# Kernel tuning notes

Hardware: AMD Instinct MI355X
Metric: run time of the kernel (lower is better)

The kernel has to match this reference:

```python
import jax, jax.numpy as jnp
import numpy as np

B, E = 256, 512
C, K = 8192, 10          # n_class, n_center
LMD = 10.0
INV_GAMMA = 10.0         # 1 / gamma, gamma = 0.1
TAU = 0.2
MARGIN = 0.01


def setup_inputs() -> dict:
    key = jax.random.key(0)
    k1, k2, k3 = jax.random.split(key, 3)
    embeddings = jax.random.normal(k1, (B, E), dtype=jnp.float32)
    labels = jax.random.randint(k2, (B,), 0, C, dtype=jnp.int64)
    fc = jax.random.normal(k3, (C * K, E), dtype=jnp.float32)
    return {"embeddings": embeddings, "labels": labels, "fc": fc}


def reference(embeddings, labels, fc):
    # L2-normalize centers (rows of fc), like F.normalize(fc, p=2, dim=1)
    norm = jnp.sqrt(jnp.sum(fc * fc, axis=1, keepdims=True))
    w = fc / jnp.maximum(norm, 1e-12)

    # similarity to every center: [B, C, K]
    x = (embeddings @ w.T).reshape(B, C, K)
    prob = jax.nn.softmax(INV_GAMMA * x, axis=2)
    h = jnp.sum(prob * x, axis=2)  # [B, C] soft-pooled class similarity

    # subtract margin on ground-truth class, then cross-entropy
    rows = jnp.arange(B)
    margin_m = jnp.zeros_like(h).at[rows, labels].set(MARGIN)
    logits = LMD * (h - margin_m)
    logp = jax.nn.log_softmax(logits, axis=1)
    loss_cls = -jnp.mean(logp[rows, labels])

    # regularizer: batched per-class center gram, replaces python loop over C
    wc = w.reshape(C, K, E)
    sub = 1.0 - jnp.einsum('cke,cje->ckj', wc, wc)   # [C, K, K]
    sub = jnp.where(sub <= 0.0, 1e-10, sub)
    mask = jnp.triu(jnp.ones((K, K), dtype=bool), k=1)  # strict upper triangle
    safe = jnp.where(mask, 2.0 * sub, 1.0)
    reg = jnp.sum(jnp.where(mask, jnp.sqrt(safe), 0.0))
    reg = reg / (C * K * (K - 1.0))
    return loss_cls + TAU * reg
```

## Files before the change

kernel.cpp:

```cpp
#include <hip/hip_runtime.h>


typedef __bf16 bf16;
typedef bf16 bf16x8 __attribute__((ext_vector_type(8)));
typedef float f32x4 __attribute__((ext_vector_type(4)));

#define NCLASS 8192
#define KC 10
#define EDIM 512
#define BATCH 256
#define BK 64

__device__ inline void load_lds16(const void* g, void* l) {
    __builtin_amdgcn_global_load_lds(
        (const __attribute__((address_space(1))) void*)g,
        (__attribute__((address_space(3))) void*)l, 16, 0, 0);
}

__global__ __launch_bounds__(256) void prep_kernel(
    const float* __restrict__ fc, bf16* __restrict__ w,
    float* __restrict__ gram_part,
    const float* __restrict__ e, bf16* __restrict__ At,
    float* __restrict__ sumexp)
{
    __shared__ float rows[KC * EDIM];
    __shared__ float s_invn[KC];
    __shared__ float s_wsum[4];
    const int t = threadIdx.x;

    if (blockIdx.x >= NCLASS) {
        if (blockIdx.x == NCLASS + 64) {
            sumexp[t] = 0.0f;
            return;
        }
        int i = (blockIdx.x - NCLASS) * 256 + t;
        int row = i >> 6, chunk = i & 63;
        int k = chunk * 8;
        float4 a = ((const float4*)e)[i * 2];
        float4 b = ((const float4*)e)[i * 2 + 1];
        bf16x8 v;
        v[0] = (bf16)a.x; v[1] = (bf16)a.y; v[2] = (bf16)a.z; v[3] = (bf16)a.w;
        v[4] = (bf16)b.x; v[5] = (bf16)b.y; v[6] = (bf16)b.z; v[7] = (bf16)b.w;
        *(bf16x8*)&At[((k >> 5) << 13) + (row << 5) + (k & 31)] = v;
        return;
    }

    const int c = blockIdx.x;
    const int wave = t >> 6, lane = t & 63;

    const float4* src = (const float4*)(fc + (size_t)c * (KC * EDIM));
    float4* rows4 = (float4*)rows;
    #pragma unroll
    for (int i = 0; i < 5; ++i) rows4[t + i * 256] = src[t + i * 256];
    __syncthreads();

    for (int r = wave; r < KC; r += 4) {
        float s = 0.f;
        #pragma unroll
        for (int j = 0; j < 8; ++j) {
            float v = rows[r * EDIM + lane + j * 64];
            s += v * v;
        }
        #pragma unroll
        for (int off = 32; off; off >>= 1) s += __shfl_xor(s, off);
        if (lane == 0) s_invn[r] = 1.0f / fmaxf(sqrtf(s), 1e-12f);
    }
    __syncthreads();

    bf16x8* dst = (bf16x8*)(w + (size_t)c * (KC * EDIM));
    #pragma unroll
    for (int p = 0; p < 3; ++p) {
        int j = t + p * 256;
        if (j < 640) {
            int r = j >> 6;
            float inv = s_invn[r];
            float4 a = *(const float4*)(rows + j * 8);
            float4 b = *(const float4*)(rows + j * 8 + 4);
            bf16x8 v;
            v[0] = (bf16)(a.x * inv); v[1] = (bf16)(a.y * inv);
            v[2] = (bf16)(a.z * inv); v[3] = (bf16)(a.w * inv);
            v[4] = (bf16)(b.x * inv); v[5] = (bf16)(b.y * inv);
            v[6] = (bf16)(b.z * inv); v[7] = (bf16)(b.w * inv);
            dst[j] = v;
        }
    }

    float part = 0.f;
    for (int p = wave; p < 45; p += 4) {
        int i = 0, pp = p;
        while (pp >= 9 - i) { pp -= 9 - i; ++i; }
        int j = i + 1 + pp;
        float s = 0.f;
        #pragma unroll
        for (int u = 0; u < 8; ++u)
            s += rows[i * EDIM + lane + u * 64] * rows[j * EDIM + lane + u * 64];
        #pragma unroll
        for (int off = 32; off; off >>= 1) s += __shfl_xor(s, off);
        if (lane == 0) {
            float sub = 1.0f - s * s_invn[i] * s_invn[j];
            if (sub <= 0.0f) sub = 1e-10f;
            part += sqrtf(2.0f * sub);
        }
    }
    if (lane == 0) s_wsum[wave] = part;
    __syncthreads();
    if (t == 0) gram_part[c] = s_wsum[0] + s_wsum[1] + s_wsum[2] + s_wsum[3];
}

__global__ __launch_bounds__(512, 2) void gemm_h_kernel(
    const bf16* __restrict__ W,
    const bf16* __restrict__ At,
    const int* __restrict__ labels,
    float* __restrict__ sumexp,
    float* __restrict__ lab_logit)
{
    __shared__ bf16 Ws[2][80 * BK];
    const int tid = threadIdx.x;
    const int wave = tid >> 6, lane = tid & 63;

    f32x4 acc[5][2];
    #pragma unroll
    for (int mt = 0; mt < 5; ++mt)
        #pragma unroll
        for (int nt = 0; nt < 2; ++nt)
            acc[mt][nt] = (f32x4){0.f, 0.f, 0.f, 0.f};

    const size_t g0 = (size_t)blockIdx.x * 80;

    const int rA = tid >> 3, sA = tid & 7;
    const bf16* srcA = W + (g0 + rA) * EDIM + ((sA ^ (rA & 7)) << 3);
    const int rB = (512 + tid) >> 3, sB = tid & 7;
    const bf16* srcB = W + (g0 + rB) * EDIM + ((sB ^ (rB & 7)) << 3);

    const int q = lane >> 4;
    const int q8 = q * 8;
    const int fr = lane & 15;

    load_lds16(srcA, &Ws[0][wave * 512]);
    if (tid < 128) load_lds16(srcB, &Ws[0][4096 + wave * 512]);
    __syncthreads();

    for (int t = 0; t < 8; ++t) {
        const int cur = t & 1;
        if (t < 7) {
            const int kb = (t + 1) * BK;
            load_lds16(srcA + kb, &Ws[cur ^ 1][wave * 512]);
            if (tid < 128) load_lds16(srcB + kb, &Ws[cur ^ 1][4096 + wave * 512]);
        }
        #pragma unroll
        for (int kk = 0; kk < BK; kk += 32) {
            const int ccb = kk >> 3;
            bf16x8 wf[5], ef[2];
            #pragma unroll
            for (int nt = 0; nt < 2; ++nt) {
                int row = wave * 32 + nt * 16 + fr;
                ef[nt] = *(const bf16x8*)
                    &At[((t * 2 + (kk >> 5)) << 13) + (row << 5) + q8];
            }
            #pragma unroll
            for (int mt = 0; mt < 5; ++mt) {
                int row = mt * 16 + fr;
                int s = (ccb + q) ^ (row & 7);
                wf[mt] = *(const bf16x8*)&Ws[cur][row * BK + (s << 3)];
            }
            #pragma unroll
            for (int mt = 0; mt < 5; ++mt)
                #pragma unroll
                for (int nt = 0; nt < 2; ++nt)
                    acc[mt][nt] = __builtin_amdgcn_mfma_f32_16x16x32_bf16(
                        wf[mt], ef[nt], acc[mt][nt], 0, 0, 0);
        }
        __syncthreads();
    }

    const int col = lane & 15;
    const int quad = lane >> 4;
    const int cb = blockIdx.x * 8;
    #pragma unroll
    for (int nt = 0; nt < 2; ++nt) {
        int b = wave * 32 + nt * 16 + col;
        float hval[8];
        #pragma unroll
        for (int cc = 0; cc < 8; ++cc) {
            float xm = -1e30f;
            #pragma unroll
            for (int mt = 0; mt < 5; ++mt) {
                if (10 * cc + 10 > 16 * mt && 10 * cc < 16 * mt + 16) {
                    #pragma unroll
                    for (int rg = 0; rg < 4; ++rg) {
                        int r = 16 * mt + 4 * quad + rg;
                        if (r >= 10 * cc && r < 10 * cc + 10)
                            xm = fmaxf(xm, acc[mt][nt][rg]);
                    }
                }
            }
            xm = fmaxf(xm, __shfl_xor(xm, 16));
            xm = fmaxf(xm, __shfl_xor(xm, 32));
            float s1 = 0.f, s2 = 0.f;
            #pragma unroll
            for (int mt = 0; mt < 5; ++mt) {
                if (10 * cc + 10 > 16 * mt && 10 * cc < 16 * mt + 16) {
                    #pragma unroll
                    for (int rg = 0; rg < 4; ++rg) {
                        int r = 16 * mt + 4 * quad + rg;
                        if (r >= 10 * cc && r < 10 * cc + 10) {
                            float x = acc[mt][nt][rg];
                            float e = __expf(10.0f * (x - xm));
                            s1 += e; s2 += e * x;
                        }
                    }
                }
            }
            s1 += __shfl_xor(s1, 16); s1 += __shfl_xor(s1, 32);
            s2 += __shfl_xor(s2, 16); s2 += __shfl_xor(s2, 32);
            hval[cc] = s2 / s1;
        }
        if (quad == 0) {
            const int lbl = labels[b];
            float ps = 0.f;
            #pragma unroll
            for (int cc = 0; cc < 8; ++cc) {
                float lg = 10.0f * hval[cc];
                if (lbl == cb + cc) {
                    lg -= 0.1f;
                    lab_logit[b] = lg;
                }
                ps += __expf(lg);
            }
            atomicAdd(&sumexp[b], ps);
        }
    }
}

__global__ __launch_bounds__(256) void final_kernel(
    const float* __restrict__ gram_part, const float* __restrict__ sumexp,
    const float* __restrict__ lab_logit, float* __restrict__ out)
{
    __shared__ float red[4];
    const int t = threadIdx.x, wave = t >> 6, lane = t & 63;
    const float4* gp4 = (const float4*)gram_part;
    float g = 0.f;
    #pragma unroll
    for (int i = 0; i < 8; ++i) {
        float4 x = gp4[t + i * 256];
        g += x.x + x.y + x.z + x.w;
    }
    float ce = logf(sumexp[t]) - lab_logit[t];
    float val = ce * (1.0f / 256.0f)
              + g * (0.2f / 737280.0f);
    #pragma unroll
    for (int off = 32; off; off >>= 1) val += __shfl_xor(val, off);
    if (lane == 0) red[wave] = val;
    __syncthreads();
    if (t == 0) out[0] = red[0] + red[1] + red[2] + red[3];
}

extern "C" void kernel_launch(void* const* d_in, const int* in_sizes, int n_in,
                              void* d_out, int out_size, void* d_ws, size_t ws_size,
                              hipStream_t stream) {
    const float* emb    = (const float*)d_in[0];
    const int*   labels = (const int*)d_in[1];
    const float* fc     = (const float*)d_in[2];
    float* out = (float*)d_out;

    char* ws = (char*)d_ws;
    bf16*  w         = (bf16*)ws;
    bf16*  At        = (bf16*)(ws + 83886080);
    float* gram_part = (float*)(ws + 84148224);
    float* sumexp    = (float*)(ws + 84181248);
    float* lab_logit = (float*)(ws + 84182272);

    prep_kernel<<<NCLASS + 65, 256, 0, stream>>>(fc, w, gram_part, emb, At,
                                                 sumexp);
    gemm_h_kernel<<<81920 / 80, 512, 0, stream>>>(w, At, labels,
                                                  sumexp, lab_logit);
    final_kernel<<<1, 256, 0, stream>>>(gram_part, sumexp, lab_logit, out);
}
```

Baseline: 304.6 us.

## Assign one class per wave in prep kernel, keep center rows in registers

The prep kernel now gives each wave its own class instead of one class per 256-thread block. Each lane holds 8 floats of all 10 rows in registers and computes the norms and all 45 Gram dot products with wave shuffles, with no shared memory or block barriers. This removes LDS staging and __syncthreads overhead and shrinks the grid by four. The cost is higher register pressure (80 floats of row data per lane) and 45 serialized shuffle reductions per wave.

```diff
diff --git a/kernel.cpp b/kernel.cpp
--- a/kernel.cpp
+++ b/kernel.cpp
@@ -23,17 +23,14 @@
     const float* __restrict__ e, bf16* __restrict__ At,
     float* __restrict__ sumexp)
 {
-    __shared__ float rows[KC * EDIM];
-    __shared__ float s_invn[KC];
-    __shared__ float s_wsum[4];
     const int t = threadIdx.x;
 
-    if (blockIdx.x >= NCLASS) {
-        if (blockIdx.x == NCLASS + 64) {
+    if (blockIdx.x >= 2048) {
+        if (blockIdx.x == 2048 + 64) {
             sumexp[t] = 0.0f;
             return;
         }
-        int i = (blockIdx.x - NCLASS) * 256 + t;
+        int i = (blockIdx.x - 2048) * 256 + t;
         int row = i >> 6, chunk = i & 63;
         int k = chunk * 8;
         float4 a = ((const float4*)e)[i * 2];
@@ -45,66 +42,58 @@
         return;
     }
 
-    const int c = blockIdx.x;
     const int wave = t >> 6, lane = t & 63;
-
-    const float4* src = (const float4*)(fc + (size_t)c * (KC * EDIM));
-    float4* rows4 = (float4*)rows;
-    #pragma unroll
-    for (int i = 0; i < 5; ++i) rows4[t + i * 256] = src[t + i * 256];
-    __syncthreads();
-
-    for (int r = wave; r < KC; r += 4) {
-        float s = 0.f;
-        #pragma unroll
-        for (int j = 0; j < 8; ++j) {
-            float v = rows[r * EDIM + lane + j * 64];
-            s += v * v;
-        }
+    const int c = blockIdx.x * 4 + wave;
+
+    float4 ra[KC][2];
+    #pragma unroll
+    for (int r = 0; r < KC; ++r) {
+        const float4* rp =
+            (const float4*)(fc + ((size_t)c * KC + r) * EDIM) + lane * 2;
+        ra[r][0] = rp[0];
+        ra[r][1] = rp[1];
+    }
+
+    float invn[KC];
+    #pragma unroll
+    for (int r = 0; r < KC; ++r) {
+        float4 a = ra[r][0], b = ra[r][1];
+        float s = a.x*a.x + a.y*a.y + a.z*a.z + a.w*a.w
+                + b.x*b.x + b.y*b.y + b.z*b.z + b.w*b.w;
         #pragma unroll
         for (int off = 32; off; off >>= 1) s += __shfl_xor(s, off);
-        if (lane == 0) s_invn[r] = 1.0f / fmaxf(sqrtf(s), 1e-12f);
-    }
-    __syncthreads();
-
-    bf16x8* dst = (bf16x8*)(w + (size_t)c * (KC * EDIM));
-    #pragma unroll
-    for (int p = 0; p < 3; ++p) {
-        int j = t + p * 256;
-        if (j < 640) {
-            int r = j >> 6;
-            float inv = s_invn[r];
-            float4 a = *(const float4*)(rows + j * 8);
-            float4 b = *(const float4*)(rows + j * 8 + 4);
-            bf16x8 v;
-            v[0] = (bf16)(a.x * inv); v[1] = (bf16)(a.y * inv);
-            v[2] = (bf16)(a.z * inv); v[3] = (bf16)(a.w * inv);
-            v[4] = (bf16)(b.x * inv); v[5] = (bf16)(b.y * inv);
-            v[6] = (bf16)(b.z * inv); v[7] = (bf16)(b.w * inv);
-            dst[j] = v;
-        }
+        invn[r] = 1.0f / fmaxf(sqrtf(s), 1e-12f);
     }
 
     float part = 0.f;
-    for (int p = wave; p < 45; p += 4) {
-        int i = 0, pp = p;
-        while (pp >= 9 - i) { pp -= 9 - i; ++i; }
-        int j = i + 1 + pp;
-        float s = 0.f;
-        #pragma unroll
-        for (int u = 0; u < 8; ++u)
-            s += rows[i * EDIM + lane + u * 64] * rows[j * EDIM + lane + u * 64];
-        #pragma unroll
-        for (int off = 32; off; off >>= 1) s += __shfl_xor(s, off);
-        if (lane == 0) {
-            float sub = 1.0f - s * s_invn[i] * s_invn[j];
+    #pragma unroll
+    for (int i = 0; i < KC - 1; ++i) {
+        #pragma unroll
+        for (int j = i + 1; j < KC; ++j) {
+            float4 ai = ra[i][0], bi = ra[i][1];
+            float4 aj = ra[j][0], bj = ra[j][1];
+            float s = ai.x*aj.x + ai.y*aj.y + ai.z*aj.z + ai.w*aj.w
+                    + bi.x*bj.x + bi.y*bj.y + bi.z*bj.z + bi.w*bj.w;
+            #pragma unroll
+            for (int off = 32; off; off >>= 1) s += __shfl_xor(s, off);
+            float sub = 1.0f - s * invn[i] * invn[j];
             if (sub <= 0.0f) sub = 1e-10f;
             part += sqrtf(2.0f * sub);
         }
     }
-    if (lane == 0) s_wsum[wave] = part;
-    __syncthreads();
-    if (t == 0) gram_part[c] = s_wsum[0] + s_wsum[1] + s_wsum[2] + s_wsum[3];
+    if (lane == 0) gram_part[c] = part;
+
+    #pragma unroll
+    for (int r = 0; r < KC; ++r) {
+        float inv = invn[r];
+        float4 a = ra[r][0], b = ra[r][1];
+        bf16x8 v;
+        v[0] = (bf16)(a.x * inv); v[1] = (bf16)(a.y * inv);
+        v[2] = (bf16)(a.z * inv); v[3] = (bf16)(a.w * inv);
+        v[4] = (bf16)(b.x * inv); v[5] = (bf16)(b.y * inv);
+        v[6] = (bf16)(b.z * inv); v[7] = (bf16)(b.w * inv);
+        *(bf16x8*)&w[((size_t)c * KC + r) * EDIM + lane * 8] = v;
+    }
 }
 
 __global__ __launch_bounds__(512, 2) void gemm_h_kernel(
@@ -270,8 +259,8 @@
     float* sumexp    = (float*)(ws + 84181248);
     float* lab_logit = (float*)(ws + 84182272);
 
-    prep_kernel<<<NCLASS + 65, 256, 0, stream>>>(fc, w, gram_part, emb, At,
-                                                 sumexp);
+    prep_kernel<<<2048 + 65, 256, 0, stream>>>(fc, w, gram_part, emb, At,
+                                               sumexp);
     gemm_h_kernel<<<81920 / 80, 512, 0, stream>>>(w, At, labels,
                                                   sumexp, lab_logit);
     final_kernel<<<1, 256, 0, stream>>>(gram_part, sumexp, lab_logit, out);
```

Result: no change. 309.4 us (+1.6%).
